# Performance work log

Measured on AMD Instinct MI355X. Metric: run time of the kernel, lower is better.

Reference implementation:

```python
import jax, jax.numpy as jnp
import numpy as np

SCALE = 8.0  # sqrt(d_k), d_k = 64


def setup_inputs() -> dict:
    key = jax.random.key(0)
    kq, kk, kv = jax.random.split(key, 3)
    B, S, D = 16, 2048, 64
    q = jax.random.normal(kq, (B, S, D), dtype=jnp.float32)
    k = jax.random.normal(kk, (B, S, D), dtype=jnp.float32)
    v = jax.random.normal(kv, (B, S, D), dtype=jnp.float32)
    # causal mask: True = masked (future positions), broadcast to batch
    causal = jnp.triu(jnp.ones((S, S), dtype=jnp.bool_), k=1)
    mask = jnp.broadcast_to(causal, (B, S, S))
    return {"q": q, "k": k, "v": v, "mask": mask}


def reference(q, k, v, mask):
    # u = (q @ k^T) / scale  -> [B, S, S]
    u = jnp.einsum("bqd,bkd->bqk", q, k) / SCALE
    u = jnp.where(mask, -jnp.inf, u)
    attn = jax.nn.softmax(u, axis=2)
    output = jnp.einsum("bqk,bkd->bqd", attn, v)
    return (attn, output)
```

## Files before the change

kernel.cpp:

```cpp
#include <hip/hip_runtime.h>
#include <hip/hip_bf16.h>

typedef __attribute__((ext_vector_type(4))) float  f32x4;
typedef __attribute__((ext_vector_type(8))) __bf16 bf16x8;
typedef __attribute__((ext_vector_type(4))) __bf16 bf16x4;

#define S_DIM 2048
#define D_DIM 64
#define A2    0.180336880f
#define TPITCH 68

__device__ __forceinline__ int swz(int r, int c) {
    return r * 64 + (c ^ ((r & 7) << 3));
}

__device__ __forceinline__ void loadK4(const float* Kb, int kt, int tid, f32x4 kr[4]) {
    #pragma unroll
    for (int i = 0; i < 4; ++i)
        kr[i] = *(const f32x4*)(Kb + (size_t)(kt * 64 + (tid >> 4) + i * 16) * D_DIM
                                + (tid & 15) * 4);
}
__device__ __forceinline__ void writeK4(__bf16* buf, int tid, const f32x4 kr[4]) {
    #pragma unroll
    for (int i = 0; i < 4; ++i) {
        bf16x4 h;
        h[0] = (__bf16)kr[i][0]; h[1] = (__bf16)kr[i][1];
        h[2] = (__bf16)kr[i][2]; h[3] = (__bf16)kr[i][3];
        *(bf16x4*)&buf[swz((tid >> 4) + i * 16, (tid & 15) * 4)] = h;
    }
}
__device__ __forceinline__ void loadQfrag(const float* Qb, int w, int c0, int jb, bf16x8 qf[2]) {
    const float* qp = Qb + (w * 16 + c0) * D_DIM + jb * 8;
    #pragma unroll
    for (int h = 0; h < 2; ++h) {
        f32x4 x0 = *(const f32x4*)(qp + h * 32);
        f32x4 x1 = *(const f32x4*)(qp + h * 32 + 4);
        bf16x8 f;
        f[0] = (__bf16)x0[0]; f[1] = (__bf16)x0[1];
        f[2] = (__bf16)x0[2]; f[3] = (__bf16)x0[3];
        f[4] = (__bf16)x1[0]; f[5] = (__bf16)x1[1];
        f[6] = (__bf16)x1[2]; f[7] = (__bf16)x1[3];
        qf[h] = f;
    }
}
__device__ __forceinline__ void mfmaS(const __bf16* bufK, const bf16x8 qf[2],
                                      int c0, int jb, f32x4 sacc[4]) {
    #pragma unroll
    for (int nt = 0; nt < 4; ++nt) sacc[nt] = (f32x4){0.f, 0.f, 0.f, 0.f};
    #pragma unroll
    for (int kk = 0; kk < 2; ++kk) {
        #pragma unroll
        for (int nt = 0; nt < 4; ++nt) {
            bf16x8 kb = *(bf16x8*)&bufK[swz(nt * 16 + c0, kk * 32 + jb * 8)];
            sacc[nt] = __builtin_amdgcn_mfma_f32_16x16x32_bf16(qf[kk], kb, sacc[nt], 0, 0, 0);
        }
    }
}

__global__ __launch_bounds__(256) void tile_pv4_kernel(
    const float* __restrict__ Q, const float* __restrict__ K,
    const float* __restrict__ V, __bf16* __restrict__ obase,
    float* __restrict__ lbase)
{
    __shared__ __attribute__((aligned(16))) __bf16 ldsK[64 * 64];
    __shared__ __attribute__((aligned(16))) __bf16 ldsV[64 * 64];
    __shared__ __attribute__((aligned(16))) __bf16 ldsP[64 * 64];

    const int tid = threadIdx.x, lane = tid & 63, w = tid >> 6;
    const int c0 = lane & 15, jb = lane >> 4;

    const int sid = ((blockIdx.x & 7) << 9) | (blockIdx.x >> 3);
    const int b = sid >> 8, qt = (sid >> 3) & 31, g = sid & 7;
    if (g * 4 > qt) return;
    const int k0 = g * 4, kend = min(k0 + 4, qt + 1);
    const int q0 = qt * 64;
    const size_t slot = (size_t)sid;

    const float* Kb = K + (size_t)b * S_DIM * D_DIM;
    const float* Vb = V + (size_t)b * S_DIM * D_DIM;

    bf16x8 qf[2];
    loadQfrag(Q + ((size_t)b * S_DIM + q0) * D_DIM, w, c0, jb, qf);

    float l2[4] = {0.f, 0.f, 0.f, 0.f};
    f32x4 oacc[4];
    #pragma unroll
    for (int nt = 0; nt < 4; ++nt) oacc[nt] = (f32x4){0.f, 0.f, 0.f, 0.f};

    for (int kt = k0; kt < kend; ++kt) {
        f32x4 kr[4];
        loadK4(Kb, kt, tid, kr);
        writeK4(ldsK, tid, kr);
        {
            float vv[16];
            #pragma unroll
            for (int i = 0; i < 16; ++i)
                vv[i] = Vb[(size_t)(kt * 64 + w * 16 + i) * D_DIM + lane];
            bf16x8 h0, h1;
            #pragma unroll
            for (int j = 0; j < 8; ++j) { h0[j] = (__bf16)vv[j]; h1[j] = (__bf16)vv[8 + j]; }
            *(bf16x8*)&ldsV[swz(lane, w * 16)]     = h0;
            *(bf16x8*)&ldsV[swz(lane, w * 16 + 8)] = h1;
        }
        __syncthreads();

        f32x4 sacc[4];
        mfmaS(ldsK, qf, c0, jb, sacc);
        const bool diag = (kt == qt);
        #pragma unroll
        for (int nt = 0; nt < 4; ++nt) {
            #pragma unroll
            for (int reg = 0; reg < 4; ++reg) {
                const int qr = w * 16 + jb * 4 + reg;
                const int kc = nt * 16 + c0;
                float p = (diag && kc > qr) ? 0.0f : exp2f(sacc[nt][reg] * A2);
                ldsP[swz(qr, kc)] = (__bf16)p;
                l2[reg] += p;
            }
        }
        #pragma unroll
        for (int kk = 0; kk < 2; ++kk) {
            bf16x8 pa = *(bf16x8*)&ldsP[swz(w * 16 + c0, kk * 32 + jb * 8)];
            #pragma unroll
            for (int nt = 0; nt < 4; ++nt) {
                bf16x8 vb = *(bf16x8*)&ldsV[swz(nt * 16 + c0, kk * 32 + jb * 8)];
                oacc[nt] = __builtin_amdgcn_mfma_f32_16x16x32_bf16(pa, vb, oacc[nt], 0, 0, 0);
            }
        }
        __syncthreads();
    }

    #pragma unroll
    for (int reg = 0; reg < 4; ++reg) {
        float l = l2[reg];
        #pragma unroll
        for (int off = 1; off < 16; off <<= 1) l += __shfl_xor(l, off);
        if (c0 == 0) lbase[slot * 64 + w * 16 + jb * 4 + reg] = l;
    }
    #pragma unroll
    for (int nt = 0; nt < 4; ++nt) {
        #pragma unroll
        for (int reg = 0; reg < 4; ++reg) {
            const int qr = w * 16 + jb * 4 + reg;
            obase[slot * 4096 + qr * 64 + nt * 16 + c0] = (__bf16)oacc[nt][reg];
        }
    }
}

__global__ __launch_bounds__(256) void merge4_kernel(
    const __bf16* __restrict__ obase, const float* __restrict__ lbase,
    float* __restrict__ out, float* __restrict__ cef)
{
    const int sid = ((blockIdx.x & 7) << 8) | (blockIdx.x >> 3);
    const int b = sid >> 7, qt = (sid >> 2) & 31, quad = sid & 3;
    const int tid = threadIdx.x;
    const int r  = quad * 16 + (tid >> 4);
    const int c4 = (tid & 15) * 4;
    const int ng = (qt >> 2) + 1;
    const size_t base = (size_t)(b * 32 + qt) * 8;

    float a0 = 0.f, a1 = 0.f, a2 = 0.f, a3 = 0.f, lsum = 0.f;
    for (int g = 0; g < ng; ++g) {
        const __bf16* op = obase + (base + g) * 4096 + r * 64 + c4;
        bf16x4 a = *(const bf16x4*)op;
        a0 += (float)a[0]; a1 += (float)a[1]; a2 += (float)a[2]; a3 += (float)a[3];
        lsum += lbase[(base + g) * 64 + r];
    }
    const float inv = 1.0f / lsum;
    f32x4 o = {a0 * inv, a1 * inv, a2 * inv, a3 * inv};
    *(f32x4*)&out[((size_t)b * S_DIM + qt * 64 + r) * D_DIM + c4] = o;
    if ((tid & 15) == 0) cef[b * S_DIM + qt * 64 + r] = -log2f(lsum);
}

__global__ __launch_bounds__(256) void attn_tile_kernel(
    const float* __restrict__ Q, const float* __restrict__ K,
    float* __restrict__ attn, const float* __restrict__ cef)
{
    __shared__ __attribute__((aligned(16))) __bf16 ldsK[64 * 64];
    __shared__ __attribute__((aligned(16))) float  ldsT[64 * TPITCH];

    const int tid = threadIdx.x, lane = tid & 63, w = tid >> 6;
    const int c0 = lane & 15, jb = lane >> 4;

    const int sid = ((blockIdx.x & 7) << 11) | (blockIdx.x >> 3);
    const int b = sid >> 10, qt = (sid >> 5) & 31, kt = sid & 31;

    float* tileP = attn + ((size_t)b * S_DIM + qt * 64) * S_DIM + kt * 64;

    if (kt > qt) {
        f32x4 z = {0.f, 0.f, 0.f, 0.f};
        #pragma unroll
        for (int i = 0; i < 4; ++i) {
            int r  = i * 16 + (tid >> 4);
            int c4 = (tid & 15) * 4;
            *(f32x4*)&tileP[(size_t)r * S_DIM + c4] = z;
        }
        return;
    }

    const float* Kb = K + ((size_t)b * S_DIM + kt * 64) * D_DIM;
    #pragma unroll
    for (int i = 0; i < 4; ++i) {
        int r  = (tid >> 4) + i * 16;
        int c4 = (tid & 15) * 4;
        f32x4 x = *(const f32x4*)(Kb + (size_t)r * D_DIM + c4);
        bf16x4 h;
        h[0] = (__bf16)x[0]; h[1] = (__bf16)x[1];
        h[2] = (__bf16)x[2]; h[3] = (__bf16)x[3];
        *(bf16x4*)&ldsK[swz(r, c4)] = h;
    }
    bf16x8 qf[2];
    loadQfrag(Q + ((size_t)b * S_DIM + qt * 64) * D_DIM, w, c0, jb, qf);
    float ce[4];
    #pragma unroll
    for (int reg = 0; reg < 4; ++reg)
        ce[reg] = cef[b * S_DIM + qt * 64 + w * 16 + jb * 4 + reg];
    __syncthreads();

    f32x4 sacc[4];
    mfmaS(ldsK, qf, c0, jb, sacc);

    const bool diag = (kt == qt);
    #pragma unroll
    for (int nt = 0; nt < 4; ++nt) {
        #pragma unroll
        for (int reg = 0; reg < 4; ++reg) {
            const int qr = w * 16 + jb * 4 + reg;
            const int kc = nt * 16 + c0;
            float p = (diag && kc > qr) ? 0.0f
                    : exp2f(fmaf(sacc[nt][reg], A2, ce[reg]));
            ldsT[qr * TPITCH + kc] = p;
        }
    }
    __syncthreads();
    #pragma unroll
    for (int i = 0; i < 4; ++i) {
        int r  = i * 16 + (tid >> 4);
        int c4 = (tid & 15) * 4;
        f32x4 x = *(f32x4*)&ldsT[r * TPITCH + c4];
        *(f32x4*)&tileP[(size_t)r * S_DIM + c4] = x;
    }
}

extern "C" void kernel_launch(void* const* d_in, const int* in_sizes, int n_in,
                              void* d_out, int out_size, void* d_ws, size_t ws_size,
                              hipStream_t stream) {
    const float* Q = (const float*)d_in[0];
    const float* K = (const float*)d_in[1];
    const float* V = (const float*)d_in[2];
    float* attn = (float*)d_out;
    float* out  = attn + (size_t)16 * S_DIM * S_DIM;

    __bf16* obase = (__bf16*)d_ws;
    float*  lbase = (float*)((char*)d_ws + (size_t)4096 * 4096 * 2);
    float*  cef   = lbase + (size_t)4096 * 64;

    tile_pv4_kernel <<<dim3(4096),  dim3(256), 0, stream>>>(Q, K, V, obase, lbase);
    merge4_kernel   <<<dim3(2048),  dim3(256), 0, stream>>>(obase, lbase, out, cef);
    attn_tile_kernel<<<dim3(16384), dim3(256), 0, stream>>>(Q, K, attn, cef);
}
```

Measured before the change: 98.40 us.

## Accumulate row sums with atomics and run output merge after attention tiles

The partial-tile kernel now accumulates softmax row sums directly into a per-row buffer with atomicAdd, so the attention-tile kernel no longer has to wait for a merge pass to produce normalizers. The O merge is moved after the attention kernel and only sums the bf16 partials. This adds a memset launch and atomic traffic, and atomic float addition makes the summation order nondeterministic. The total kernel count stays similar, but the attention kernel now computes log2 itself.

```diff
diff --git a/kernel.cpp b/kernel.cpp
--- a/kernel.cpp
+++ b/kernel.cpp
@@ -57,10 +57,10 @@
     }
 }
 
-__global__ __launch_bounds__(256) void tile_pv4_kernel(
+__global__ __launch_bounds__(256) void tile_pv4a_kernel(
     const float* __restrict__ Q, const float* __restrict__ K,
     const float* __restrict__ V, __bf16* __restrict__ obase,
-    float* __restrict__ lbase)
+    float* __restrict__ lsum)
 {
     __shared__ __attribute__((aligned(16))) __bf16 ldsK[64 * 64];
     __shared__ __attribute__((aligned(16))) __bf16 ldsV[64 * 64];
@@ -135,7 +135,8 @@
         float l = l2[reg];
         #pragma unroll
         for (int off = 1; off < 16; off <<= 1) l += __shfl_xor(l, off);
-        if (c0 == 0) lbase[slot * 64 + w * 16 + jb * 4 + reg] = l;
+        if (c0 == 0)
+            atomicAdd(&lsum[b * S_DIM + q0 + w * 16 + jb * 4 + reg], l);
     }
     #pragma unroll
     for (int nt = 0; nt < 4; ++nt) {
@@ -147,34 +148,9 @@
     }
 }
 
-__global__ __launch_bounds__(256) void merge4_kernel(
-    const __bf16* __restrict__ obase, const float* __restrict__ lbase,
-    float* __restrict__ out, float* __restrict__ cef)
-{
-    const int sid = ((blockIdx.x & 7) << 8) | (blockIdx.x >> 3);
-    const int b = sid >> 7, qt = (sid >> 2) & 31, quad = sid & 3;
-    const int tid = threadIdx.x;
-    const int r  = quad * 16 + (tid >> 4);
-    const int c4 = (tid & 15) * 4;
-    const int ng = (qt >> 2) + 1;
-    const size_t base = (size_t)(b * 32 + qt) * 8;
-
-    float a0 = 0.f, a1 = 0.f, a2 = 0.f, a3 = 0.f, lsum = 0.f;
-    for (int g = 0; g < ng; ++g) {
-        const __bf16* op = obase + (base + g) * 4096 + r * 64 + c4;
-        bf16x4 a = *(const bf16x4*)op;
-        a0 += (float)a[0]; a1 += (float)a[1]; a2 += (float)a[2]; a3 += (float)a[3];
-        lsum += lbase[(base + g) * 64 + r];
-    }
-    const float inv = 1.0f / lsum;
-    f32x4 o = {a0 * inv, a1 * inv, a2 * inv, a3 * inv};
-    *(f32x4*)&out[((size_t)b * S_DIM + qt * 64 + r) * D_DIM + c4] = o;
-    if ((tid & 15) == 0) cef[b * S_DIM + qt * 64 + r] = -log2f(lsum);
-}
-
 __global__ __launch_bounds__(256) void attn_tile_kernel(
     const float* __restrict__ Q, const float* __restrict__ K,
-    float* __restrict__ attn, const float* __restrict__ cef)
+    float* __restrict__ attn, const float* __restrict__ lsum)
 {
     __shared__ __attribute__((aligned(16))) __bf16 ldsK[64 * 64];
     __shared__ __attribute__((aligned(16))) float  ldsT[64 * TPITCH];
@@ -214,7 +190,7 @@
     float ce[4];
     #pragma unroll
     for (int reg = 0; reg < 4; ++reg)
-        ce[reg] = cef[b * S_DIM + qt * 64 + w * 16 + jb * 4 + reg];
+        ce[reg] = -log2f(lsum[b * S_DIM + qt * 64 + w * 16 + jb * 4 + reg]);
     __syncthreads();
 
     f32x4 sacc[4];
@@ -240,6 +216,29 @@
         f32x4 x = *(f32x4*)&ldsT[r * TPITCH + c4];
         *(f32x4*)&tileP[(size_t)r * S_DIM + c4] = x;
     }
+}
+
+__global__ __launch_bounds__(256) void mergeO_kernel(
+    const __bf16* __restrict__ obase, const float* __restrict__ lsum,
+    float* __restrict__ out)
+{
+    const int sid = ((blockIdx.x & 7) << 8) | (blockIdx.x >> 3);
+    const int b = sid >> 7, qt = (sid >> 2) & 31, quad = sid & 3;
+    const int tid = threadIdx.x;
+    const int r  = quad * 16 + (tid >> 4);
+    const int c4 = (tid & 15) * 4;
+    const int ng = (qt >> 2) + 1;
+    const size_t base = (size_t)(b * 256 + qt * 8);
+
+    float a0 = 0.f, a1 = 0.f, a2 = 0.f, a3 = 0.f;
+    for (int g = 0; g < ng; ++g) {
+        const __bf16* op = obase + (base + g) * 4096 + r * 64 + c4;
+        bf16x4 a = *(const bf16x4*)op;
+        a0 += (float)a[0]; a1 += (float)a[1]; a2 += (float)a[2]; a3 += (float)a[3];
+    }
+    const float inv = 1.0f / lsum[b * S_DIM + qt * 64 + r];
+    f32x4 o = {a0 * inv, a1 * inv, a2 * inv, a3 * inv};
+    *(f32x4*)&out[((size_t)b * S_DIM + qt * 64 + r) * D_DIM + c4] = o;
 }
 
 extern "C" void kernel_launch(void* const* d_in, const int* in_sizes, int n_in,
@@ -252,10 +251,10 @@
     float* out  = attn + (size_t)16 * S_DIM * S_DIM;
 
     __bf16* obase = (__bf16*)d_ws;
-    float*  lbase = (float*)((char*)d_ws + (size_t)4096 * 4096 * 2);
-    float*  cef   = lbase + (size_t)4096 * 64;
-
-    tile_pv4_kernel <<<dim3(4096),  dim3(256), 0, stream>>>(Q, K, V, obase, lbase);
-    merge4_kernel   <<<dim3(2048),  dim3(256), 0, stream>>>(obase, lbase, out, cef);
-    attn_tile_kernel<<<dim3(16384), dim3(256), 0, stream>>>(Q, K, attn, cef);
-}
+    float*  lsum  = (float*)((char*)d_ws + (size_t)4096 * 4096 * 2);
+
+    hipMemsetAsync(lsum, 0, (size_t)16 * S_DIM * sizeof(float), stream);
+    tile_pv4a_kernel<<<dim3(4096),  dim3(256), 0, stream>>>(Q, K, V, obase, lsum);
+    attn_tile_kernel<<<dim3(16384), dim3(256), 0, stream>>>(Q, K, attn, lsum);
+    mergeO_kernel   <<<dim3(2048),  dim3(256), 0, stream>>>(obase, lsum, out);
+}
```

After: 99.77 us. No clear change (+1.4%).
